# Kernel tuning notes

Measured on AMD Instinct MI355X. Metric: run time of the kernel, lower is better.

The kernel has to match this reference:

```python
import jax, jax.numpy as jnp
import numpy as np

N = 50000      # nodes
E = 800000     # edges (before self-loops)
F_IN = 128     # input features
HID = 64       # hidden width
CLS = 40       # classes
NEG_SLOPE = 0.2  # PyG GATConv default
EPS = 1e-16


def setup_inputs() -> dict:
    key = jax.random.key(0)
    ks = jax.random.split(key, 16)

    def lin(k, fi, fo):
        return jax.random.normal(k, (fi, fo), jnp.float32) / np.float32(np.sqrt(fi))

    def att(k, f):
        return jax.random.normal(k, (f,), jnp.float32) / np.float32(np.sqrt(f))

    return {
        "x": jax.random.normal(ks[0], (N, F_IN), jnp.float32),
        "edge_index": jax.random.randint(ks[1], (2, E), 0, N, dtype=jnp.int64),
        "W1": lin(ks[2], F_IN, HID), "a_src1": att(ks[3], HID), "a_dst1": att(ks[4], HID), "b1": jnp.zeros((HID,), jnp.float32),
        "W2": lin(ks[5], HID, HID),  "a_src2": att(ks[6], HID), "a_dst2": att(ks[7], HID), "b2": jnp.zeros((HID,), jnp.float32),
        "W3": lin(ks[8], HID, CLS),  "a_src3": att(ks[9], CLS), "a_dst3": att(ks[10], CLS), "b3": jnp.zeros((CLS,), jnp.float32),
    }


def gat_layer(x, src, dst, W, a_src, a_dst, b, n):
    # Single-head GATConv (PyG semantics, heads=1, add_self_loops already applied).
    h = x @ W                                  # [n, out]
    s_src = h @ a_src                          # [n]
    s_dst = h @ a_dst                          # [n]
    e = jax.nn.leaky_relu(s_src[src] + s_dst[dst], NEG_SLOPE)  # [E']
    # softmax over incoming edges of each destination node
    m = jax.ops.segment_max(e, dst, num_segments=n)            # [n]
    e = jnp.exp(e - m[dst])
    denom = jax.ops.segment_sum(e, dst, num_segments=n)        # [n]
    alpha = e / (denom[dst] + EPS)                             # [E']
    out = jax.ops.segment_sum(h[src] * alpha[:, None], dst, num_segments=n)
    return out + b


def reference(x, edge_index, W1, a_src1, a_dst1, b1, W2, a_src2, a_dst2, b2, W3, a_src3, a_dst3, b3):
    n = x.shape[0]
    loop = jnp.arange(n, dtype=edge_index.dtype)
    src = jnp.concatenate([edge_index[0], loop])   # add self-loops (GATConv default)
    dst = jnp.concatenate([edge_index[1], loop])

    h = gat_layer(x, src, dst, W1, a_src1, a_dst1, b1, n)
    h = jax.nn.gelu(h, approximate=False)          # torch F.gelu default = exact erf
    h = gat_layer(h, src, dst, W2, a_src2, a_dst2, b2, n)
    h = jax.nn.gelu(h, approximate=False)
    out = gat_layer(h, src, dst, W3, a_src3, a_dst3, b3, n)
    return out
```

## Files before the change

### kernel.cpp

```cpp
#include <hip/hip_runtime.h>
#include <hip/hip_bf16.h>
#include <math.h>


#define PAD_CAP 64

__device__ __forceinline__ int detect64(const int* __restrict__ ei) {
  int any = 0;
#pragma unroll
  for (int i = 1; i < 64; i += 2) any |= ei[i];
  return any == 0;
}

__device__ __forceinline__ void load_edge(const int* __restrict__ ei, int E,
                                          int e, int is64, int n, int& s,
                                          int& d) {
  if (is64) {
    s = ei[2 * e];
    d = ei[2 * (E + e)];
  } else {
    s = ei[e];
    d = ei[E + e];
  }
  s = min(max(s, 0), n - 1);
  d = min(max(d, 0), n - 1);
}

__global__ void scatter_padded(const int* __restrict__ ei, int E, int n,
                               int* __restrict__ deg, int* __restrict__ col) {
  const int is64 = detect64(ei);
  const int e = blockIdx.x * blockDim.x + threadIdx.x;
  if (e >= E + n) return;
  int s, d;
  if (e < E) load_edge(ei, E, e, is64, n, s, d);
  else s = d = e - E;
  const int pos = atomicAdd(deg + d, 1);
  if (pos < PAD_CAP) col[((size_t)d << 6) + pos] = s;
}


template <int F_IN, int F_OUT>
__global__ __launch_bounds__(256) void gemm_att(
    const float* __restrict__ x, const float* __restrict__ W,
    const float* __restrict__ a_src, const float* __restrict__ a_dst,
    __hip_bfloat16* __restrict__ h, float* __restrict__ s_src,
    float* __restrict__ s_dst, int n) {
  constexpr int TF = F_OUT / 4;
  __shared__ float Xt[F_IN * 65];
  __shared__ float red[2][4][64];
  const int wave = threadIdx.x >> 6, lane = threadIdx.x & 63;
  const int nb0 = blockIdx.x * 64;
  const int node = nb0 + lane;

  {
    constexpr int Q = F_IN / 4;
    for (int i = threadIdx.x; i < 64 * Q; i += 256) {
      const int nd = i / Q, k4 = i % Q;
      float4 v = {0.f, 0.f, 0.f, 0.f};
      if (nb0 + nd < n)
        v = *(const float4*)(x + (size_t)(nb0 + nd) * F_IN + 4 * k4);
      Xt[(4 * k4 + 0) * 65 + nd] = v.x;
      Xt[(4 * k4 + 1) * 65 + nd] = v.y;
      Xt[(4 * k4 + 2) * 65 + nd] = v.z;
      Xt[(4 * k4 + 3) * 65 + nd] = v.w;
    }
  }
  __syncthreads();

  const int f0 = __builtin_amdgcn_readfirstlane(wave * TF);
  float acc[TF];
#pragma unroll
  for (int ff = 0; ff < TF; ++ff) acc[ff] = 0.f;

#pragma unroll 4
  for (int k = 0; k < F_IN; ++k) {
    const float xk = Xt[k * 65 + lane];
#pragma unroll
    for (int ff = 0; ff < TF; ++ff)
      acc[ff] = fmaf(xk, W[k * F_OUT + f0 + ff], acc[ff]);
  }

  float pa = 0.f, pb = 0.f;
#pragma unroll
  for (int ff = 0; ff < TF; ++ff) {
    pa = fmaf(acc[ff], a_src[f0 + ff], pa);
    pb = fmaf(acc[ff], a_dst[f0 + ff], pb);
  }
  if (node < n) {
#pragma unroll
    for (int ff = 0; ff < TF; ++ff)
      h[(size_t)node * F_OUT + f0 + ff] = __float2bfloat16(acc[ff]);
  }
  red[0][wave][lane] = pa;
  red[1][wave][lane] = pb;
  __syncthreads();
  if (wave == 0 && node < n) {
    s_src[node] = red[0][0][lane] + red[0][1][lane] + red[0][2][lane] +
                  red[0][3][lane];
    s_dst[node] = red[1][0][lane] + red[1][1][lane] + red[1][2][lane] +
                  red[1][3][lane];
  }
}

template <int F_OUT, bool GELU>
__global__ __launch_bounds__(256) void attn_aggr(
    const int* __restrict__ col, const int* __restrict__ deg_arr,
    const float* __restrict__ ssrc, const float* __restrict__ sdst,
    const __hip_bfloat16* __restrict__ h, const float* __restrict__ bias,
    float* __restrict__ out, int n) {
  const int wave = threadIdx.x >> 6, lane = threadIdx.x & 63;
  const int d = blockIdx.x * 4 + wave;
  if (d >= n) return;
  const int beg = d << 6;
  const int deg = min(deg_arr[d], PAD_CAP);
  const float sd = sdst[d];

  int s0 = 0;
  float v0 = 0.f, m = -INFINITY;
  if (lane < deg) {
    s0 = col[beg + lane];
    float t = ssrc[s0] + sd;
    v0 = t > 0.f ? t : 0.2f * t;
    m = v0;
  }
#pragma unroll
  for (int off = 32; off > 0; off >>= 1) m = fmaxf(m, __shfl_xor(m, off));

  const float w0 = (lane < deg) ? __expf(v0 - m) : 0.f;
  float den = w0;
#pragma unroll
  for (int off = 32; off > 0; off >>= 1) den += __shfl_xor(den, off);
  const float inv = 1.f / (den + 1e-16f);

  const __hip_bfloat16* hl = h + lane;
  float acc = 0.f;
  const int dmain = deg;
  int i = 0;
  for (; i + 16 <= dmain; i += 16) {
    int ss[16];
    float ww[16], hh[16];
#pragma unroll
    for (int j = 0; j < 16; ++j) {
      ss[j] = __shfl(s0, i + j);
      ww[j] = __shfl(w0, i + j);
    }
    if (lane < F_OUT) {
#pragma unroll
      for (int j = 0; j < 16; ++j)
        hh[j] = __bfloat162float(hl[(size_t)ss[j] * F_OUT]);
    } else {
#pragma unroll
      for (int j = 0; j < 16; ++j) hh[j] = 0.f;
    }
#pragma unroll
    for (int j = 0; j < 16; ++j) acc = fmaf(ww[j], hh[j], acc);
  }
  for (; i + 4 <= dmain; i += 4) {
    int ss[4];
    float ww[4], hh[4];
#pragma unroll
    for (int j = 0; j < 4; ++j) {
      ss[j] = __shfl(s0, i + j);
      ww[j] = __shfl(w0, i + j);
    }
    if (lane < F_OUT) {
#pragma unroll
      for (int j = 0; j < 4; ++j)
        hh[j] = __bfloat162float(hl[(size_t)ss[j] * F_OUT]);
    } else {
#pragma unroll
      for (int j = 0; j < 4; ++j) hh[j] = 0.f;
    }
#pragma unroll
    for (int j = 0; j < 4; ++j) acc = fmaf(ww[j], hh[j], acc);
  }
  for (; i < dmain; ++i) {
    const int s = __shfl(s0, i);
    const float wi = __shfl(w0, i);
    if (lane < F_OUT)
      acc = fmaf(wi, __bfloat162float(hl[(size_t)s * F_OUT]), acc);
  }

  if (lane < F_OUT) {
    float v = acc * inv + bias[lane];
    if (GELU) v = 0.5f * v * (1.0f + erff(v * 0.70710678118654752f));
    out[(size_t)d * F_OUT + lane] = v;
  }
}

extern "C" void kernel_launch(void* const* d_in, const int* in_sizes, int n_in,
                              void* d_out, int out_size, void* d_ws,
                              size_t ws_size, hipStream_t stream) {
  const float* x = (const float*)d_in[0];
  const int* ei = (const int*)d_in[1];
  const float* W1 = (const float*)d_in[2];
  const float* as1 = (const float*)d_in[3];
  const float* ad1 = (const float*)d_in[4];
  const float* b1 = (const float*)d_in[5];
  const float* W2 = (const float*)d_in[6];
  const float* as2 = (const float*)d_in[7];
  const float* ad2 = (const float*)d_in[8];
  const float* b2 = (const float*)d_in[9];
  const float* W3 = (const float*)d_in[10];
  const float* as3 = (const float*)d_in[11];
  const float* ad3 = (const float*)d_in[12];
  const float* b3 = (const float*)d_in[13];

  const int n = in_sizes[0] / 128;
  const int E = in_sizes[1] / 2;
  const int total = E + n;

  const size_t need = ((size_t)n * (32 + 64 + 1 + 1 + 1 + PAD_CAP)) * 4 + 256;
  if (ws_size < need) return;

  __hip_bfloat16* hb = (__hip_bfloat16*)d_ws;
  float* B = (float*)d_ws + (size_t)n * 32;
  float* ssrc = B + (size_t)n * 64;
  float* sdst = ssrc + n;
  int* deg = (int*)(sdst + n);
  int* col = deg + n;

  const int tb = (total + 255) / 256;
  const int gemm_blocks = (n + 63) / 64;
  const int aggr_blocks = (n + 3) / 4;

  hipMemsetAsync(deg, 0, (size_t)n * 4, stream);
  scatter_padded<<<tb, 256, 0, stream>>>(ei, E, n, deg, col);

  gemm_att<128, 64><<<gemm_blocks, 256, 0, stream>>>(x, W1, as1, ad1, hb, ssrc,
                                                     sdst, n);
  attn_aggr<64, true><<<aggr_blocks, 256, 0, stream>>>(col, deg, ssrc, sdst,
                                                       hb, b1, B, n);

  gemm_att<64, 64><<<gemm_blocks, 256, 0, stream>>>(B, W2, as2, ad2, hb, ssrc,
                                                    sdst, n);
  attn_aggr<64, true><<<aggr_blocks, 256, 0, stream>>>(col, deg, ssrc, sdst,
                                                       hb, b2, B, n);

  gemm_att<64, 40><<<gemm_blocks, 256, 0, stream>>>(B, W3, as3, ad3, hb, ssrc,
                                                    sdst, n);
  attn_aggr<40, false><<<aggr_blocks, 256, 0, stream>>>(
      col, deg, ssrc, sdst, hb, b3, (float*)d_out, n);
}
```

Before: 307.6 us.

## Vectorize neighbor gathers into quad-edge uint2 loads and fuse edge scatter into first GEMM

The aggregation kernel now assigns 16 lanes per edge, each loading 4 bf16 features with one 8-byte load, processing 4 edges in parallel per wave and reducing across quads with shuffles. Output and bias are written as float4. The CSR-padding scatter is folded into the first GEMM kernel with a grid-stride loop and batched atomics, removing a separate launch. This cuts gather instruction count but adds cross-quad reductions and makes the first GEMM kernel heavier.

```diff
diff --git a/kernel.cpp b/kernel.cpp
--- a/kernel.cpp
+++ b/kernel.cpp
@@ -26,25 +26,47 @@
   d = min(max(d, 0), n - 1);
 }
 
-__global__ void scatter_padded(const int* __restrict__ ei, int E, int n,
-                               int* __restrict__ deg, int* __restrict__ col) {
-  const int is64 = detect64(ei);
-  const int e = blockIdx.x * blockDim.x + threadIdx.x;
-  if (e >= E + n) return;
-  int s, d;
-  if (e < E) load_edge(ei, E, e, is64, n, s, d);
-  else s = d = e - E;
-  const int pos = atomicAdd(deg + d, 1);
-  if (pos < PAD_CAP) col[((size_t)d << 6) + pos] = s;
-}
-
-
-template <int F_IN, int F_OUT>
+
+template <int F_IN, int F_OUT, bool SCATTER>
 __global__ __launch_bounds__(256) void gemm_att(
     const float* __restrict__ x, const float* __restrict__ W,
     const float* __restrict__ a_src, const float* __restrict__ a_dst,
     __hip_bfloat16* __restrict__ h, float* __restrict__ s_src,
-    float* __restrict__ s_dst, int n) {
+    float* __restrict__ s_dst, int n, const int* __restrict__ ei, int E,
+    int* __restrict__ deg, int* __restrict__ col) {
+  if constexpr (SCATTER) {
+    const int is64 = detect64(ei);
+    const int total = E + n;
+    const int stride = gridDim.x * blockDim.x;
+    int e = blockIdx.x * blockDim.x + threadIdx.x;
+    int sv[5], dv[5], va[5], pos[5];
+#pragma unroll
+    for (int j = 0; j < 5; ++j) {
+      va[j] = (e < total);
+      int s = 0, d = 0;
+      if (va[j]) {
+        if (e < E) load_edge(ei, E, e, is64, n, s, d);
+        else { s = e - E; d = e - E; }
+      }
+      sv[j] = s;
+      dv[j] = d;
+      e += stride;
+    }
+#pragma unroll
+    for (int j = 0; j < 5; ++j)
+      pos[j] = va[j] ? atomicAdd(deg + dv[j], 1) : PAD_CAP;
+#pragma unroll
+    for (int j = 0; j < 5; ++j)
+      if (va[j] && pos[j] < PAD_CAP) col[((size_t)dv[j] << 6) + pos[j]] = sv[j];
+    for (; e < total; e += stride) {
+      int s, d;
+      if (e < E) load_edge(ei, E, e, is64, n, s, d);
+      else { s = e - E; d = e - E; }
+      const int p = atomicAdd(deg + d, 1);
+      if (p < PAD_CAP) col[((size_t)d << 6) + p] = s;
+    }
+  }
+
   constexpr int TF = F_OUT / 4;
   __shared__ float Xt[F_IN * 65];
   __shared__ float red[2][4][64];
@@ -108,6 +130,7 @@
     const float* __restrict__ ssrc, const float* __restrict__ sdst,
     const __hip_bfloat16* __restrict__ h, const float* __restrict__ bias,
     float* __restrict__ out, int n) {
+  constexpr int NF4 = (F_OUT + 3) / 4;
   const int wave = threadIdx.x >> 6, lane = threadIdx.x & 63;
   const int d = blockIdx.x * 4 + wave;
   if (d >= n) return;
@@ -119,72 +142,82 @@
   float v0 = 0.f, m = -INFINITY;
   if (lane < deg) {
     s0 = col[beg + lane];
-    float t = ssrc[s0] + sd;
+    const float t = ssrc[s0] + sd;
     v0 = t > 0.f ? t : 0.2f * t;
     m = v0;
   }
 #pragma unroll
   for (int off = 32; off > 0; off >>= 1) m = fmaxf(m, __shfl_xor(m, off));
-
   const float w0 = (lane < deg) ? __expf(v0 - m) : 0.f;
   float den = w0;
 #pragma unroll
   for (int off = 32; off > 0; off >>= 1) den += __shfl_xor(den, off);
   const float inv = 1.f / (den + 1e-16f);
 
-  const __hip_bfloat16* hl = h + lane;
-  float acc = 0.f;
-  const int dmain = deg;
+  const int q = lane >> 4, t4 = lane & 15;
+  const bool act = (t4 < NF4);
+  const unsigned short* __restrict__ hu = (const unsigned short*)h + 4 * t4;
+
+  float ax = 0.f, ay = 0.f, az = 0.f, aw = 0.f;
   int i = 0;
-  for (; i + 16 <= dmain; i += 16) {
-    int ss[16];
-    float ww[16], hh[16];
-#pragma unroll
-    for (int j = 0; j < 16; ++j) {
-      ss[j] = __shfl(s0, i + j);
-      ww[j] = __shfl(w0, i + j);
-    }
-    if (lane < F_OUT) {
-#pragma unroll
-      for (int j = 0; j < 16; ++j)
-        hh[j] = __bfloat162float(hl[(size_t)ss[j] * F_OUT]);
-    } else {
-#pragma unroll
-      for (int j = 0; j < 16; ++j) hh[j] = 0.f;
-    }
-#pragma unroll
-    for (int j = 0; j < 16; ++j) acc = fmaf(ww[j], hh[j], acc);
-  }
-  for (; i + 4 <= dmain; i += 4) {
+  for (; i + 16 <= deg; i += 16) {
     int ss[4];
-    float ww[4], hh[4];
+    float ww[4];
+    uint2 hv[4];
 #pragma unroll
     for (int j = 0; j < 4; ++j) {
-      ss[j] = __shfl(s0, i + j);
-      ww[j] = __shfl(w0, i + j);
-    }
-    if (lane < F_OUT) {
-#pragma unroll
-      for (int j = 0; j < 4; ++j)
-        hh[j] = __bfloat162float(hl[(size_t)ss[j] * F_OUT]);
-    } else {
-#pragma unroll
-      for (int j = 0; j < 4; ++j) hh[j] = 0.f;
-    }
-#pragma unroll
-    for (int j = 0; j < 4; ++j) acc = fmaf(ww[j], hh[j], acc);
-  }
-  for (; i < dmain; ++i) {
-    const int s = __shfl(s0, i);
-    const float wi = __shfl(w0, i);
-    if (lane < F_OUT)
-      acc = fmaf(wi, __bfloat162float(hl[(size_t)s * F_OUT]), acc);
-  }
-
-  if (lane < F_OUT) {
-    float v = acc * inv + bias[lane];
-    if (GELU) v = 0.5f * v * (1.0f + erff(v * 0.70710678118654752f));
-    out[(size_t)d * F_OUT + lane] = v;
+      ss[j] = __shfl(s0, i + 4 * j + q);
+      ww[j] = __shfl(w0, i + 4 * j + q);
+    }
+#pragma unroll
+    for (int j = 0; j < 4; ++j) {
+      hv[j].x = 0u;
+      hv[j].y = 0u;
+      if (act) hv[j] = *(const uint2*)(hu + (size_t)ss[j] * F_OUT);
+    }
+#pragma unroll
+    for (int j = 0; j < 4; ++j) {
+      ax = fmaf(ww[j], __uint_as_float(hv[j].x << 16), ax);
+      ay = fmaf(ww[j], __uint_as_float(hv[j].x & 0xffff0000u), ay);
+      az = fmaf(ww[j], __uint_as_float(hv[j].y << 16), az);
+      aw = fmaf(ww[j], __uint_as_float(hv[j].y & 0xffff0000u), aw);
+    }
+  }
+  for (; i < deg; i += 4) {
+    const int ss = __shfl(s0, i + q);
+    const float ww = __shfl(w0, i + q);
+    uint2 hv;
+    hv.x = 0u;
+    hv.y = 0u;
+    if (act) hv = *(const uint2*)(hu + (size_t)ss * F_OUT);
+    ax = fmaf(ww, __uint_as_float(hv.x << 16), ax);
+    ay = fmaf(ww, __uint_as_float(hv.x & 0xffff0000u), ay);
+    az = fmaf(ww, __uint_as_float(hv.y << 16), az);
+    aw = fmaf(ww, __uint_as_float(hv.y & 0xffff0000u), aw);
+  }
+
+#pragma unroll
+  for (int off = 32; off >= 16; off >>= 1) {
+    ax += __shfl_xor(ax, off);
+    ay += __shfl_xor(ay, off);
+    az += __shfl_xor(az, off);
+    aw += __shfl_xor(aw, off);
+  }
+
+  if (lane < NF4) {
+    const float4 bv = *(const float4*)(bias + 4 * lane);
+    float r0 = ax * inv + bv.x;
+    float r1 = ay * inv + bv.y;
+    float r2 = az * inv + bv.z;
+    float r3 = aw * inv + bv.w;
+    if (GELU) {
+      r0 = 0.5f * r0 * (1.f + erff(r0 * 0.70710678118654752f));
+      r1 = 0.5f * r1 * (1.f + erff(r1 * 0.70710678118654752f));
+      r2 = 0.5f * r2 * (1.f + erff(r2 * 0.70710678118654752f));
+      r3 = 0.5f * r3 * (1.f + erff(r3 * 0.70710678118654752f));
+    }
+    *(float4*)(out + (size_t)d * F_OUT + 4 * lane) =
+        make_float4(r0, r1, r2, r3);
   }
 }
 
@@ -208,7 +241,6 @@
 
   const int n = in_sizes[0] / 128;
   const int E = in_sizes[1] / 2;
-  const int total = E + n;
 
   const size_t need = ((size_t)n * (32 + 64 + 1 + 1 + 1 + PAD_CAP)) * 4 + 256;
   if (ws_size < need) return;
@@ -220,25 +252,22 @@
   int* deg = (int*)(sdst + n);
   int* col = deg + n;
 
-  const int tb = (total + 255) / 256;
   const int gemm_blocks = (n + 63) / 64;
   const int aggr_blocks = (n + 3) / 4;
 
   hipMemsetAsync(deg, 0, (size_t)n * 4, stream);
-  scatter_padded<<<tb, 256, 0, stream>>>(ei, E, n, deg, col);
-
-  gemm_att<128, 64><<<gemm_blocks, 256, 0, stream>>>(x, W1, as1, ad1, hb, ssrc,
-                                                     sdst, n);
+  gemm_att<128, 64, true><<<gemm_blocks, 256, 0, stream>>>(
+      x, W1, as1, ad1, hb, ssrc, sdst, n, ei, E, deg, col);
   attn_aggr<64, true><<<aggr_blocks, 256, 0, stream>>>(col, deg, ssrc, sdst,
                                                        hb, b1, B, n);
 
-  gemm_att<64, 64><<<gemm_blocks, 256, 0, stream>>>(B, W2, as2, ad2, hb, ssrc,
-                                                    sdst, n);
+  gemm_att<64, 64, false><<<gemm_blocks, 256, 0, stream>>>(
+      B, W2, as2, ad2, hb, ssrc, sdst, n, nullptr, 0, nullptr, nullptr);
   attn_aggr<64, true><<<aggr_blocks, 256, 0, stream>>>(col, deg, ssrc, sdst,
                                                        hb, b2, B, n);
 
-  gemm_att<64, 40><<<gemm_blocks, 256, 0, stream>>>(B, W3, as3, ad3, hb, ssrc,
-                                                    sdst, n);
+  gemm_att<64, 40, false><<<gemm_blocks, 256, 0, stream>>>(
+      B, W3, as3, ad3, hb, ssrc, sdst, n, nullptr, 0, nullptr, nullptr);
   attn_aggr<40, false><<<aggr_blocks, 256, 0, stream>>>(
       col, deg, ssrc, sdst, hb, b3, (float*)d_out, n);
 }
```

Measured after the change: 283.3 us. 7.9% less time.
